# Kernel optimization log

Hardware: AMD Instinct MI355X
Metric: run time of the kernel (lower is better)

The kernel has to match this reference:

```python
import jax, jax.numpy as jnp
import numpy as np

CONF_THRES = 0.25
IOU_THRES = 0.45
MAX_DET = 300      # max detections returned (padded/masked to static shape)
K = 8192           # top-K score candidates entering NMS (static bound)
N_ANCHORS = 102000 # YOLOv5 @ 1280px
NC = 80            # COCO classes


def setup_inputs() -> dict:
    key = jax.random.key(0)
    # [B=1, N, 4 (xywh) + 1 (obj) + 80 (cls)] raw head predictions in [0,1)
    preds = jax.random.uniform(key, (1, N_ANCHORS, 4 + 1 + NC), dtype=jnp.float32)
    return {"preds": preds}


def _xywh2yxyx(b):
    # (xc, yc, w, h) -> (y1, x1, y2, x2), matching pt_xywh2yxyx_yolo
    x, y, w, h = b[..., 0], b[..., 1], b[..., 2], b[..., 3]
    return jnp.stack([y - h * 0.5, x - w * 0.5, y + h * 0.5, x + w * 0.5], axis=-1)


def _iou_matrix(boxes):
    # boxes: [K, 4] in yxyx; returns pairwise IoU [K, K]
    area = (boxes[:, 2] - boxes[:, 0]) * (boxes[:, 3] - boxes[:, 1])
    ty = jnp.maximum(boxes[:, None, 0], boxes[None, :, 0])
    tx = jnp.maximum(boxes[:, None, 1], boxes[None, :, 1])
    by = jnp.minimum(boxes[:, None, 2], boxes[None, :, 2])
    bx = jnp.minimum(boxes[:, None, 3], boxes[None, :, 3])
    inter = jnp.clip(by - ty, 0.0) * jnp.clip(bx - tx, 0.0)
    union = area[:, None] + area[None, :] - inter
    return inter / (union + 1e-9)


def _yolo_nms(preds):
    p = preds[0]                       # [N, 85] (loop returns on first image)
    obj = p[:, 4]                      # objectness
    cand = obj > CONF_THRES            # confidence filter
    cls_scores = p[:, 5:] * obj[:, None]
    scores = jnp.max(cls_scores, axis=1)
    classes = jnp.argmax(cls_scores, axis=1).astype(jnp.float32)
    scores = jnp.where(cand, scores, 0.0)  # mask instead of dynamic filter
    boxes = _xywh2yxyx(p[:, :4])       # [N, 4] yxyx

    # top-K candidates by score (static replacement for boolean filtering)
    top_scores, idx = jax.lax.top_k(scores, K)
    top_boxes = boxes[idx]
    top_classes = classes[idx]
    valid = top_scores > 0.0

    iou = _iou_matrix(top_boxes)       # [K, K], 256 MB fp32

    # greedy NMS: boxes already sorted by descending score
    ar = jnp.arange(K)

    def body(i, suppressed):
        keep_i = jnp.logical_and(jnp.logical_not(suppressed[i]), valid[i])
        return suppressed | (keep_i & (iou[i] > IOU_THRES) & (ar > i))

    suppressed = jax.lax.fori_loop(0, K, body, jnp.zeros((K,), jnp.bool_))
    keep = valid & jnp.logical_not(suppressed)

    # gather top MAX_DET kept detections (sorted), zero-pad the rest
    keep_scores = jnp.where(keep, top_scores, -1.0)
    _, sel = jax.lax.top_k(keep_scores, MAX_DET)
    mask = keep[sel]
    out_boxes = jnp.where(mask[:, None], top_boxes[sel], 0.0)[None]    # [1, MAX_DET, 4]
    out_classes = jnp.where(mask, top_classes[sel], 0.0)[None]         # [1, MAX_DET]
    out_scores = jnp.where(mask, top_scores[sel], 0.0)[None]           # [1, MAX_DET]
    return out_boxes, out_classes, out_scores


def reference(preds):
    return _yolo_nms(preds)
```

## Files before the change

### kernel.cpp

```cpp
#include <hip/hip_runtime.h>
#include <cstdint>

#define CONF_THRES 0.25f
#define IOU_THRES  0.45f
#define MAX_DET    300
#define K_TOP      8192
#define NA         102000
#define NCLS       80
#define ROWLEN     85
#define CAP        32640
#define NPLANE     4
#define NBINS      16384
#define WIN        512
#define NWIN       (K_TOP / WIN)
#define SSTR       9

typedef unsigned long long u64;
typedef unsigned int u32;

__global__ __launch_bounds__(256) void zero_kernel(uint4* __restrict__ a,
        uint4* __restrict__ r, uint4* __restrict__ b) {
    int i = blockIdx.x * 256 + threadIdx.x;
    uint4 z = make_uint4(0u, 0u, 0u, 0u);
    if (i < 4164) a[i] = z;
    if (i < 8160) r[i] = z;
    b[i] = z;
}

__global__ __launch_bounds__(256) void score_key_kernel(const float* __restrict__ preds,
        u64* __restrict__ keys, u32* __restrict__ histP, float4* __restrict__ recs) {
#pragma clang fp contract(off)
    int lane = threadIdx.x & 63;
    int i = blockIdx.x * 4 + (threadIdx.x >> 6);
    if (i >= NA) return;
    const float* p = preds + (size_t)i * ROWLEN;
    float v0 = p[lane];
    float v1 = (lane < ROWLEN - 64) ? p[64 + lane] : 0.0f;
    float obj = __shfl(v0, 4);
    u64 kb = 0;
    if (lane >= 5) {
        float q = v0 * obj;
        kb = ((u64)__float_as_uint(q) << 8) | (u32)(255 - (lane - 5));
    }
    if (lane < 21) {
        float q = v1 * obj;
        u64 kb2 = ((u64)__float_as_uint(q) << 8) | (u32)(255 - (59 + lane));
        if (kb2 > kb) kb = kb2;
    }
    for (int off = 32; off; off >>= 1) {
        u64 o = __shfl_xor(kb, off);
        if (o > kb) kb = o;
    }
    float x = __shfl(v0, 0), y = __shfl(v0, 1);
    float w = __shfl(v0, 2), h = __shfl(v0, 3);
    if (lane == 0) {
        float maxq = __uint_as_float((u32)(kb >> 8));
        float score = (obj > CONF_THRES) ? maxq : 0.0f;
        u32 sb = __float_as_uint(score);
        u32 cls = 255u - (u32)(kb & 0xffull);
        float ymin = y - h * 0.5f, xmin = x - w * 0.5f;
        float ymax = y + h * 0.5f, xmax = x + w * 0.5f;
        keys[i] = ((u64)sb << 32) | (u32)(~(u32)i);
        recs[2 * i]     = make_float4(ymin, xmin, ymax, xmax);
        recs[2 * i + 1] = make_float4(score, (float)cls,
                                      (ymax - ymin) * (xmax - xmin), 0.0f);
        if (sb != 0u)
            atomicAdd(&histP[((u32)blockIdx.x & (NPLANE - 1u)) * NBINS + (sb >> 16)], 1u);
    }
}

__global__ __launch_bounds__(1024) void cutoff_kernel(const u32* __restrict__ histP,
        u32* __restrict__ meta) {
    __shared__ u32 suf[1024];
    __shared__ int cbs;
    __shared__ u32 above_s;
    int t = threadIdx.x;
    u32 s = 0;
    for (int r = 0; r < NPLANE; ++r) {
        const u32* hb = histP + r * NBINS + t * 16;
        for (int b = 0; b < 16; ++b) s += hb[b];
    }
    suf[t] = s;
    if (t == 0) { cbs = -1; above_s = 0; }
    __syncthreads();
    for (int off = 1; off < 1024; off <<= 1) {
        u32 add = (t + off < 1024) ? suf[t + off] : 0u;
        __syncthreads();
        suf[t] += add;
        __syncthreads();
    }
    u32 st = suf[t];
    u32 stn = (t < 1023) ? suf[t + 1] : 0u;
    if (st >= (u32)K_TOP && stn < (u32)K_TOP) {
        cbs = t;
        above_s = stn;
    }
    __syncthreads();
    int cb = cbs;
    if (t < 64) {
        u32 thresh = 0;
        if (cb >= 0) {
            u32 above = above_s;
            u32 v = 0;
            if (t < 16) {
                for (int r = 0; r < NPLANE; ++r) v += histP[r * NBINS + cb * 16 + t];
            }
            for (int off = 1; off < 64; off <<= 1) {
                u32 o = __shfl_down(v, off);
                if (t + off < 64) v += o;
            }
            u64 bal = __ballot(v + above >= (u32)K_TOP);
            int bstar = 63 - __builtin_clzll((unsigned long long)bal);
            thresh = ((u32)(cb * 16 + bstar)) << 16;
        }
        if (t == 0) meta[1] = thresh;
    }
}

__global__ __launch_bounds__(256) void compact_kernel(const u64* __restrict__ keys,
        u32* __restrict__ meta, u64* __restrict__ comp) {
    __shared__ u32 woff[4];
    __shared__ u32 bbase;
    int i = blockIdx.x * 256 + threadIdx.x;
    int wid = threadIdx.x >> 6, lane = threadIdx.x & 63;
    u64 key = (i < NA) ? keys[i] : 0ull;
    u32 sb = (u32)(key >> 32);
    u32 th = meta[1];
    bool take = (i < NA) && (sb != 0u) && (sb >= th);
    u64 bal = __ballot(take);
    if (lane == 0) woff[wid] = (u32)__popcll(bal);
    __syncthreads();
    if (threadIdx.x == 0) {
        u32 t0 = woff[0], t1 = woff[1], t2 = woff[2], t3 = woff[3];
        bbase = atomicAdd(&meta[0], t0 + t1 + t2 + t3);
        woff[0] = 0; woff[1] = t0; woff[2] = t0 + t1; woff[3] = t0 + t1 + t2;
    }
    __syncthreads();
    if (take) {
        u32 pos = bbase + woff[wid] + (u32)__popcll(bal & ((1ull << lane) - 1ull));
        if (pos < CAP) comp[pos] = key;
    }
}

__global__ __launch_bounds__(256) void rank_partial_kernel(const u64* __restrict__ comp,
        const u32* __restrict__ meta, u32* __restrict__ rankArr) {
    __shared__ u64 tile[1024];
    u32 cnt = meta[0];
    int n = (int)(cnt < (u32)CAP ? cnt : (u32)CAP);
    int i0 = blockIdx.x * 256;
    int j0 = blockIdx.y * 1024;
    if (i0 >= n || j0 >= n) return;
    int lim = n - j0; if (lim > 1024) lim = 1024;
    for (int k = threadIdx.x; k < 1024; k += 256)
        tile[k] = (k < lim) ? comp[j0 + k] : 0ull;
    __syncthreads();
    int i = i0 + threadIdx.x;
    if (i < n) {
        u64 key = comp[i];
        u32 r = 0;
#pragma unroll 8
        for (int j = 0; j < 1024; ++j) r += (tile[j] > key) ? 1u : 0u;
        atomicAdd(&rankArr[i], r);
    }
}

__global__ __launch_bounds__(256) void scatter_kernel(const u64* __restrict__ comp,
        const u32* __restrict__ meta, const u32* __restrict__ rankArr,
        u64* __restrict__ sorted) {
    u32 cnt = meta[0];
    int n = (int)(cnt < (u32)CAP ? cnt : (u32)CAP);
    int i = blockIdx.x * 256 + threadIdx.x;
    if (i < n) {
        u32 r = rankArr[i];
        if (r < (u32)K_TOP) sorted[r] = comp[i];
    }
}

__global__ __launch_bounds__(256) void gather_kernel(const u64* __restrict__ sorted,
        const float4* __restrict__ recs, float* __restrict__ boxes,
        float* __restrict__ scores, float* __restrict__ classes,
        float* __restrict__ areas) {
    int i = blockIdx.x * 256 + threadIdx.x;
    u64 key = sorted[i];
    u32 sb = (u32)(key >> 32);
    float score = __uint_as_float(sb);
    float4 b = make_float4(0.0f, 0.0f, 0.0f, 0.0f);
    float c = 0.0f, a = 0.0f;
    if (score > 0.0f) {
        u32 idx = ~(u32)(key & 0xffffffffull);
        float4 r0 = recs[2 * idx];
        float4 r1 = recs[2 * idx + 1];
        b = r0; c = r1.y; a = r1.z;
    }
    ((float4*)boxes)[i] = b;
    scores[i] = score;
    classes[i] = c;
    areas[i] = a;
}

__global__ __launch_bounds__(256) void mask_kernel(const float* __restrict__ boxes,
        const float* __restrict__ areas, const float* __restrict__ scores,
        u64* __restrict__ mask, u64* __restrict__ remw) {
#pragma clang fp contract(off)
    int cx = blockIdx.x;
    int ry = blockIdx.y;
    if (cx < (ry >> 2)) return;
    __shared__ float4 cb[256];
    __shared__ float  ca[256];
    __shared__ u64 st[64 * 5];
    int tid = threadIdx.x;
    int wv = tid >> 6, lane = tid & 63;
    int r0 = ry * 64;
    int jw = cx * 4 + wv;
    cb[tid] = ((const float4*)boxes)[cx * 256 + tid];
    ca[tid] = areas[cx * 256 + tid];
    if (cx == (ry >> 2) && wv == 0) {
        u64 b = __ballot(scores[r0 + lane] > 0.0f);
        if (lane == 0) remw[ry] = b;
    }
    __syncthreads();
    u64 myword = 0;
    if (jw >= ry) {
        float4 bi = ((const float4*)boxes)[r0 + lane];
        float ai = areas[r0 + lane];
        const double Bd = (double)IOU_THRES + 0x1p-26;
        int kb = wv * 64;
#pragma unroll
        for (int k = 0; k < 64; ++k) {
            float4 bj = cb[kb + k];
            float aj = ca[kb + k];
            float ty = fmaxf(bi.x, bj.x);
            float tx = fmaxf(bi.y, bj.y);
            float by = fminf(bi.z, bj.z);
            float bx = fminf(bi.w, bj.w);
            float inter = fmaxf(by - ty, 0.0f) * fmaxf(bx - tx, 0.0f);
            float uni = (ai + aj) - inter;
            float u = uni + 1e-9f;
            bool sup = ((double)inter > Bd * (double)u);
            myword |= sup ? (1ull << k) : 0ull;
        }
        if (jw == ry)
            myword &= (lane < 63) ? (~0ull << (lane + 1)) : 0ull;
    }
    st[lane * 5 + wv] = myword;
    __syncthreads();
    mask[(size_t)(r0 + (tid >> 2)) * 128 + cx * 4 + (tid & 3)] =
            st[(tid >> 2) * 5 + (tid & 3)];
}

__device__ __forceinline__ u64 rfl64(u64 v) {
    u32 lo = (u32)__builtin_amdgcn_readfirstlane((int)(u32)v);
    u32 hi = (u32)__builtin_amdgcn_readfirstlane((int)(u32)(v >> 32));
    return ((u64)hi << 32) | lo;
}

__device__ __forceinline__ u64 bcast64(u64 v, int srclane) {
    u32 lo = (u32)__builtin_amdgcn_readlane((int)(u32)v, srclane);
    u32 hi = (u32)__builtin_amdgcn_readlane((int)(u32)(v >> 32), srclane);
    return ((u64)hi << 32) | lo;
}

__device__ __forceinline__ u64 shfl_xor64(u64 v, int m) {
    u32 lo = __shfl_xor((u32)v, m, 64);
    u32 hi = __shfl_xor((u32)(v >> 32), m, 64);
    return ((u64)hi << 32) | lo;
}

__global__ __launch_bounds__(256) void nms_scan_kernel(const u64* __restrict__ mask,
        const u64* __restrict__ remw, const float* __restrict__ boxes,
        const float* __restrict__ scores, const float* __restrict__ classes,
        float* __restrict__ out) {
    __shared__ u64 sub[2][WIN * SSTR];
    __shared__ u32 supLo[128], supHi[128];
    __shared__ u64 rem_s[128];
    __shared__ u32 ki[MAX_DET + 8];
    __shared__ int n_sh, n0_sh;
    int tid = threadIdx.x;
    int wid = tid >> 6, lane = tid & 63;
    if (tid == 0) { n_sh = 0; n0_sh = 0; }
    if (tid < 128) { supLo[tid] = 0; supHi[tid] = 0; rem_s[tid] = remw[tid]; }
#pragma unroll
    for (int it = 0; it < 8; ++it) {
        int idx = it * 256 + tid;
        int r = idx >> 2, j = (idx & 3) * 2;
        uint4 v = *(const uint4*)&mask[(size_t)r * 128 + j];
        sub[0][r * SSTR + j]     = ((u64)v.y << 32) | v.x;
        sub[0][r * SSTR + j + 1] = ((u64)v.w << 32) | v.z;
    }
    __syncthreads();
    int n = 0;
    for (int win = 0; win < NWIN; ++win) {
        if (n >= MAX_DET) break;
        int rbase = win * WIN;
        int cb = win & 1;
        if (wid == 0) {
            u64 diag[8];
#pragma unroll
            for (int sw = 0; sw < 8; ++sw)
                diag[sw] = sub[cb][(sw * 64 + lane) * SSTR + sw];
            int n0 = n;
            u64 keptW[8] = {0, 0, 0, 0, 0, 0, 0, 0};
#pragma unroll
            for (int sw = 0; sw < 8; ++sw) {
                if (n < MAX_DET) {
                    u64 acc2 = 0;
#pragma unroll
                    for (int wp = 0; wp < 8; ++wp) {
                        if (wp < sw) {
                            if ((keptW[wp] >> lane) & 1ull)
                                acc2 |= sub[cb][(wp * 64 + lane) * SSTR + sw];
                        }
                    }
                    for (int off = 32; off; off >>= 1) acc2 |= shfl_xor64(acc2, off);
                    u64 supw = ((u64)supHi[win * 8 + sw] << 32) | supLo[win * 8 + sw];
                    u64 cur = rfl64(rem_s[win * 8 + sw]) & ~rfl64(supw) & ~rfl64(acc2);
                    u64 kw = 0;
                    while (cur != 0ull && n < MAX_DET) {
                        int b = __ffsll((unsigned long long)cur) - 1;
                        u64 slice = bcast64(diag[sw], b);
                        kw |= (1ull << b);
                        cur &= ~(slice | (1ull << b));
                        ++n;
                    }
                    keptW[sw] = kw;
                }
            }
            int base = n0;
#pragma unroll
            for (int sw = 0; sw < 8; ++sw) {
                u64 kw = keptW[sw];
                if ((kw >> lane) & 1ull) {
                    int rr = (int)__popcll(kw & ((1ull << lane) - 1ull));
                    ki[base + rr] = (u32)(rbase + sw * 64 + lane);
                }
                base += (int)__popcll(kw);
            }
            if (lane == 0) { n0_sh = n0; n_sh = n; }
        } else if (win + 1 < NWIN) {
            int t = tid - 64;
            for (int it = 0; it < 11; ++it) {
                int idx = it * 192 + t;
                if (idx < 2048) {
                    int r = idx >> 2, j = (idx & 3) * 2;
                    uint4 v = *(const uint4*)&mask[
                            (size_t)(rbase + WIN + r) * 128 + (win + 1) * 8 + j];
                    sub[cb ^ 1][r * SSTR + j]     = ((u64)v.y << 32) | v.x;
                    sub[cb ^ 1][r * SSTR + j + 1] = ((u64)v.w << 32) | v.z;
                }
            }
        }
        __syncthreads();
        int n0 = n0_sh;
        n = n_sh;
        int q = n - n0;
        if (q > 0 && n < MAX_DET && win + 1 < NWIN) {
            int total = q << 7;
            for (int idx = tid; idx < total; idx += 256) {
                int m = n0 + (idx >> 7);
                int word = idx & 127;
                u64 v = mask[(size_t)ki[m] * 128 + word];
                atomicOr(&supLo[word], (u32)v);
                atomicOr(&supHi[word], (u32)(v >> 32));
            }
        }
        __syncthreads();
    }
    __syncthreads();
    for (int m = tid; m < MAX_DET; m += 256) {
        float4 b = make_float4(0.0f, 0.0f, 0.0f, 0.0f);
        float c = 0.0f, s = 0.0f;
        if (m < n) {
            int k = (int)ki[m];
            b = ((const float4*)boxes)[k];
            c = classes[k];
            s = scores[k];
        }
        ((float4*)out)[m] = b;
        out[1200 + m] = c;
        out[1500 + m] = s;
    }
}

extern "C" void kernel_launch(void* const* d_in, const int* in_sizes, int n_in,
                              void* d_out, int out_size, void* d_ws, size_t ws_size,
                              hipStream_t stream) {
    const float* preds = (const float*)d_in[0];
    char* ws = (char*)d_ws;

    u32*   rankArr = (u32*)(ws + 65536);
    u32*   meta    = (u32*)(ws + 262144);
    u64*   remw    = (u64*)(ws + 262208);
    u64*   sorted  = (u64*)(ws + 263232);
    u64*   keys    = (u64*)(ws + 328768);
    u64*   comp    = (u64*)(ws + 1144768);
    float* tareas  = (float*)(ws + 1144768);
    float* tboxes  = (float*)(ws + 1405888);
    float* tscores = (float*)(ws + 1536960);
    float* tclass  = (float*)(ws + 1569728);
    u64*   mask    = (u64*)(ws + 1602496);
    u32*   histP   = (u32*)(ws + 1602496);
    float4* recs   = (float4*)(ws + 2126784);
    float* out     = (float*)d_out;

    zero_kernel<<<64, 256, 0, stream>>>((uint4*)(ws + 262144), (uint4*)rankArr,
            (uint4*)histP);
    score_key_kernel<<<(NA + 3) / 4, 256, 0, stream>>>(preds, keys, histP, recs);
    cutoff_kernel<<<1, 1024, 0, stream>>>(histP, meta);
    compact_kernel<<<(NA + 255) / 256, 256, 0, stream>>>(keys, meta, comp);
    rank_partial_kernel<<<dim3((CAP + 255) / 256, (CAP + 1023) / 1024), 256, 0, stream>>>(
            comp, meta, rankArr);
    scatter_kernel<<<(CAP + 255) / 256, 256, 0, stream>>>(comp, meta, rankArr, sorted);
    gather_kernel<<<K_TOP / 256, 256, 0, stream>>>(sorted, recs, tboxes, tscores,
            tclass, tareas);
    mask_kernel<<<dim3(32, 128), 256, 0, stream>>>(tboxes, tareas, tscores, mask, remw);
    nms_scan_kernel<<<1, 256, 0, stream>>>(mask, remw, tboxes, tscores, tclass, out);
}
```

Before: 238.1 us.

## Push intra-window suppression via LDS atomics and batch mask loads in NMS scan

Replaces the per-subword pull of suppression bits (masked loads plus a 64-lane shuffle reduction) with a push model: after a 64-row subword is resolved, kept lanes atomically OR their rows into small shared accumulators for later subwords. The prefetch of the next window's mask tile now issues all global loads before any shared-memory stores, exposing more memory-level parallelism. The cross-window suppression update skips words belonging to already-processed windows and unrolls four loads ahead of the atomics. This shortens the serial single-wave critical path, at the cost of more LDS atomic traffic and more registers.

```diff
diff --git a/kernel.cpp b/kernel.cpp
--- a/kernel.cpp
+++ b/kernel.cpp
@@ -260,18 +260,13 @@
     return ((u64)hi << 32) | lo;
 }
 
-__device__ __forceinline__ u64 shfl_xor64(u64 v, int m) {
-    u32 lo = __shfl_xor((u32)v, m, 64);
-    u32 hi = __shfl_xor((u32)(v >> 32), m, 64);
-    return ((u64)hi << 32) | lo;
-}
-
 __global__ __launch_bounds__(256) void nms_scan_kernel(const u64* __restrict__ mask,
         const u64* __restrict__ remw, const float* __restrict__ boxes,
         const float* __restrict__ scores, const float* __restrict__ classes,
         float* __restrict__ out) {
     __shared__ u64 sub[2][WIN * SSTR];
     __shared__ u32 supLo[128], supHi[128];
+    __shared__ u32 winLo[8], winHi[8];
     __shared__ u64 rem_s[128];
     __shared__ u32 ki[MAX_DET + 8];
     __shared__ int n_sh, n0_sh;
@@ -294,6 +289,7 @@
         int rbase = win * WIN;
         int cb = win & 1;
         if (wid == 0) {
+            if (lane < 8) { winLo[lane] = 0; winHi[lane] = 0; }
             u64 diag[8];
 #pragma unroll
             for (int sw = 0; sw < 8; ++sw)
@@ -303,17 +299,9 @@
 #pragma unroll
             for (int sw = 0; sw < 8; ++sw) {
                 if (n < MAX_DET) {
-                    u64 acc2 = 0;
-#pragma unroll
-                    for (int wp = 0; wp < 8; ++wp) {
-                        if (wp < sw) {
-                            if ((keptW[wp] >> lane) & 1ull)
-                                acc2 |= sub[cb][(wp * 64 + lane) * SSTR + sw];
-                        }
-                    }
-                    for (int off = 32; off; off >>= 1) acc2 |= shfl_xor64(acc2, off);
+                    u64 wsup = ((u64)winHi[sw] << 32) | winLo[sw];
                     u64 supw = ((u64)supHi[win * 8 + sw] << 32) | supLo[win * 8 + sw];
-                    u64 cur = rfl64(rem_s[win * 8 + sw]) & ~rfl64(supw) & ~rfl64(acc2);
+                    u64 cur = rfl64(rem_s[win * 8 + sw]) & ~rfl64(supw) & ~rfl64(wsup);
                     u64 kw = 0;
                     while (cur != 0ull && n < MAX_DET) {
                         int b = __ffsll((unsigned long long)cur) - 1;
@@ -323,6 +311,14 @@
                         ++n;
                     }
                     keptW[sw] = kw;
+                    if (sw < 7 && kw != 0ull && ((kw >> lane) & 1ull)) {
+#pragma unroll
+                        for (int wp = sw + 1; wp < 8; ++wp) {
+                            u64 v = sub[cb][(sw * 64 + lane) * SSTR + wp];
+                            atomicOr(&winLo[wp], (u32)v);
+                            atomicOr(&winHi[wp], (u32)(v >> 32));
+                        }
+                    }
                 }
             }
             int base = n0;
@@ -338,14 +334,23 @@
             if (lane == 0) { n0_sh = n0; n_sh = n; }
         } else if (win + 1 < NWIN) {
             int t = tid - 64;
+            uint4 vb[11];
+#pragma unroll
             for (int it = 0; it < 11; ++it) {
                 int idx = it * 192 + t;
                 if (idx < 2048) {
                     int r = idx >> 2, j = (idx & 3) * 2;
-                    uint4 v = *(const uint4*)&mask[
+                    vb[it] = *(const uint4*)&mask[
                             (size_t)(rbase + WIN + r) * 128 + (win + 1) * 8 + j];
-                    sub[cb ^ 1][r * SSTR + j]     = ((u64)v.y << 32) | v.x;
-                    sub[cb ^ 1][r * SSTR + j + 1] = ((u64)v.w << 32) | v.z;
+                }
+            }
+#pragma unroll
+            for (int it = 0; it < 11; ++it) {
+                int idx = it * 192 + t;
+                if (idx < 2048) {
+                    int r = idx >> 2, j = (idx & 3) * 2;
+                    sub[cb ^ 1][r * SSTR + j]     = ((u64)vb[it].y << 32) | vb[it].x;
+                    sub[cb ^ 1][r * SSTR + j + 1] = ((u64)vb[it].w << 32) | vb[it].z;
                 }
             }
         }
@@ -354,13 +359,25 @@
         n = n_sh;
         int q = n - n0;
         if (q > 0 && n < MAX_DET && win + 1 < NWIN) {
+            int wbase = (win + 1) * 8;
             int total = q << 7;
-            for (int idx = tid; idx < total; idx += 256) {
-                int m = n0 + (idx >> 7);
-                int word = idx & 127;
-                u64 v = mask[(size_t)ki[m] * 128 + word];
-                atomicOr(&supLo[word], (u32)v);
-                atomicOr(&supHi[word], (u32)(v >> 32));
+            for (int b0 = tid; b0 < total; b0 += 256 * 4) {
+                u64 v[4]; int wd[4]; bool ok[4];
+#pragma unroll
+                for (int u = 0; u < 4; ++u) {
+                    int idx = b0 + u * 256;
+                    wd[u] = idx & 127;
+                    ok[u] = (idx < total) && (wd[u] >= wbase);
+                    int m = ok[u] ? (n0 + (idx >> 7)) : n0;
+                    v[u] = ok[u] ? mask[(size_t)ki[m] * 128 + wd[u]] : 0ull;
+                }
+#pragma unroll
+                for (int u = 0; u < 4; ++u) {
+                    if (ok[u]) {
+                        atomicOr(&supLo[wd[u]], (u32)v[u]);
+                        atomicOr(&supHi[wd[u]], (u32)(v[u] >> 32));
+                    }
+                }
             }
         }
         __syncthreads();
```

After: 302.8 us. 27.2% more time.
